# Optimization experiments

Hardware: AMD Instinct MI355X
Metric: run time of the kernel (lower is better)

Reference implementation:

```python
import jax, jax.numpy as jnp
import numpy as np

MIDC = 128
HEADS = 4
HEADC = MIDC // HEADS
EPS = 1e-5


def _layernorm(x, w, b):
    # Faithful to the custom torch LayerNorm: unbiased std (ddof=1) and (std + eps) in denominator.
    mean = jnp.mean(x, axis=-1, keepdims=True)
    std = jnp.std(x, axis=-1, keepdims=True, ddof=1)
    return w * ((x - mean) / (std + EPS)) + b


def setup_inputs() -> dict:
    key = jax.random.key(0)
    ks = jax.random.split(key, 8)
    B, C, D, H, W = 2, MIDC, 16, 64, 64
    s = 1.0 / np.sqrt(C)
    return {
        "x": jax.random.normal(ks[0], (B, C, D, H, W), dtype=jnp.float32),
        "qkv_w": jax.random.normal(ks[1], (3 * C, C), dtype=jnp.float32) * s,
        "qkv_b": jnp.zeros((3 * C,), dtype=jnp.float32),
        "o1_w": jax.random.normal(ks[2], (C, C), dtype=jnp.float32) * s,
        "o1_b": jnp.zeros((C,), dtype=jnp.float32),
        "o2_w": jax.random.normal(ks[3], (C, C), dtype=jnp.float32) * s,
        "o2_b": jnp.zeros((C,), dtype=jnp.float32),
        "kln_w": jnp.ones((HEADS, 1, HEADC), dtype=jnp.float32),
        "kln_b": jnp.zeros((HEADS, 1, HEADC), dtype=jnp.float32),
        "vln_w": jnp.ones((HEADS, 1, HEADC), dtype=jnp.float32),
        "vln_b": jnp.zeros((HEADS, 1, HEADC), dtype=jnp.float32),
    }


def reference(x, qkv_w, qkv_b, o1_w, o1_b, o2_w, o2_b, kln_w, kln_b, vln_w, vln_b):
    B, C, D, H, W = x.shape
    heads, headc = HEADS, HEADC
    bias = x
    # 1x1x1 Conv3d == pointwise linear over channel dim
    qkv = jnp.einsum('bcdhw,oc->bdhwo', x, qkv_w) + qkv_b          # [B,D,H,W,3C]
    qkv = qkv.reshape(B * D, H * W, heads, 3 * headc)
    qkv = qkv.transpose(0, 2, 1, 3)                                 # [BD,heads,HW,3hc]
    q, k, v = jnp.split(qkv, 3, axis=-1)                            # each [BD,heads,HW,hc]
    k = _layernorm(k, kln_w, kln_b)
    v = _layernorm(v, vln_w, vln_b)
    # linear attention: (K^T V) then Q (K^T V)
    kv = jnp.einsum('bhnc,bhnd->bhcd', k, v) / (H * W)              # [BD,heads,hc,hc]
    v = jnp.einsum('bhnc,bhcd->bhnd', q, kv)                        # [BD,heads,HW,hc]
    v = v.transpose(0, 2, 1, 3).reshape(B, D, H, W, C)
    ret = v.transpose(0, 4, 1, 2, 3) + bias                         # [B,C,D,H,W]
    h = jnp.einsum('bcdhw,oc->bodhw', ret, o1_w) + o1_b[None, :, None, None, None]
    h = jax.nn.gelu(h, approximate=False)
    out = jnp.einsum('bcdhw,oc->bodhw', h, o2_w) + o2_b[None, :, None, None, None]
    return out + bias
```

## Files before the change

### kernel.cpp

```cpp
#include <hip/hip_runtime.h>
#include <cmath>

typedef float  f32x4  __attribute__((ext_vector_type(4)));
typedef __bf16 bf16x8 __attribute__((ext_vector_type(8)));
typedef __bf16 bf16x4 __attribute__((ext_vector_type(4)));

#define MFMA16(acc, a, b) (acc) = __builtin_amdgcn_mfma_f32_16x16x32_bf16((a), (b), (acc), 0, 0, 0)


__device__ __forceinline__ int swz(int row, int colByte){ return row*256 + (colByte ^ ((row & 7) << 4)); }
__device__ __forceinline__ int swzP(int row, int colByte){ return row*128 + (colByte ^ ((row & 7) << 4)); }

__device__ __forceinline__ void loadx(float* sx, const float* __restrict__ xb, int t){
  int p = t & 63, cg = t >> 6;
  const float* col = xb + p;
  #pragma unroll
  for (int i = 0; i < 4; ++i)
    #pragma unroll
    for (int j = 0; j < 8; ++j)
      sx[i*8 + j] = col[(cg*8 + i*32 + j) * 65536];
}
__device__ __forceinline__ void writex(const float* sx, char* ldsX, int t){
  int p = t & 63, cg = t >> 6;
  #pragma unroll
  for (int i = 0; i < 4; ++i){
    bf16x8 u;
    #pragma unroll
    for (int j = 0; j < 8; ++j) u[j] = (__bf16)sx[i*8 + j];
    *(bf16x8*)(ldsX + swz(p, cg*16 + i*64)) = u;
  }
}

__global__ __launch_bounds__(256) void wprep(const float* __restrict__ qkv_w,
                                             const float* __restrict__ o1w,
                                             const float* __restrict__ o2w,
                                             __bf16* __restrict__ w16){
  int e = (blockIdx.x * 256 + threadIdx.x) * 4;
  const float* src; int off;
  if (e < 49152)      { src = qkv_w; off = e; }
  else if (e < 65536) { src = o1w;   off = e - 49152; }
  else                { src = o2w;   off = e - 65536; }
  f32x4 v = *(const f32x4*)(src + off);
  bf16x4 o;
  #pragma unroll
  for (int r = 0; r < 4; ++r) o[r] = (__bf16)v[r];
  *(bf16x4*)(w16 + e) = o;
}

__global__ __launch_bounds__(256, 5) void k1_kv(
    const float* __restrict__ x, const __bf16* __restrict__ w16, const float* __restrict__ qkv_b,
    const float* __restrict__ klw, const float* __restrict__ klb,
    const float* __restrict__ vlw, const float* __restrict__ vlb,
    float* __restrict__ kvacc){
  __shared__ char ldsX[16384];
  __shared__ char ksS[4][4096];
  int t = threadIdx.x, lane = t & 63, w = t >> 6, l15 = lane & 15, l4 = lane >> 4;
  int bx = blockIdx.x, bd = bx >> 6, b = bd >> 4, d = bd & 15;
  const float* xb = x + (size_t)b*8388608 + d*4096 + (bx & 63)*64;

  float sx[32];
  loadx(sx, xb, t);
  writex(sx, ldsX, t);
  __syncthreads();

  char* ks = ksS[w];
  f32x4 accv[2][4];
  #pragma unroll
  for (int ph = 0; ph < 2; ++ph){
    int po = 96*w + 32 + 32*ph;
    f32x4 acc[2][4] = {};
    #pragma unroll
    for (int kf = 0; kf < 4; ++kf){
      bf16x8 a0 = *(const bf16x8*)(w16 + (po + l15)*128 + kf*32 + l4*8);
      bf16x8 a1 = *(const bf16x8*)(w16 + (po + 16 + l15)*128 + kf*32 + l4*8);
      bf16x8 bn0 = *(const bf16x8*)(ldsX + swz(l15,      kf*64 + l4*16));
      bf16x8 bn1 = *(const bf16x8*)(ldsX + swz(16 + l15, kf*64 + l4*16));
      bf16x8 bn2 = *(const bf16x8*)(ldsX + swz(32 + l15, kf*64 + l4*16));
      bf16x8 bn3 = *(const bf16x8*)(ldsX + swz(48 + l15, kf*64 + l4*16));
      MFMA16(acc[0][0], a0, bn0); MFMA16(acc[0][1], a0, bn1);
      MFMA16(acc[0][2], a0, bn2); MFMA16(acc[0][3], a0, bn3);
      MFMA16(acc[1][0], a1, bn0); MFMA16(acc[1][1], a1, bn1);
      MFMA16(acc[1][2], a1, bn2); MFMA16(acc[1][3], a1, bn3);
    }
    const float* lwp = (ph ? vlw : klw) + 32*w;
    const float* lbp = (ph ? vlb : klb) + 32*w;
    f32x4 b0  = *(const f32x4*)(qkv_b + po + l4*4);
    f32x4 b1  = *(const f32x4*)(qkv_b + po + 16 + l4*4);
    f32x4 lw0 = *(const f32x4*)(lwp + l4*4), lw1 = *(const f32x4*)(lwp + 16 + l4*4);
    f32x4 lb0 = *(const f32x4*)(lbp + l4*4), lb1 = *(const f32x4*)(lbp + 16 + l4*4);
    #pragma unroll
    for (int n = 0; n < 4; ++n){
      f32x4 v0 = acc[0][n] + b0;
      f32x4 v1 = acc[1][n] + b1;
      float s1 = v0[0]+v0[1]+v0[2]+v0[3] + v1[0]+v1[1]+v1[2]+v1[3];
      float s2 = v0[0]*v0[0]+v0[1]*v0[1]+v0[2]*v0[2]+v0[3]*v0[3]
               + v1[0]*v1[0]+v1[1]*v1[1]+v1[2]*v1[2]+v1[3]*v1[3];
      s1 += __shfl_xor(s1, 16); s2 += __shfl_xor(s2, 16);
      s1 += __shfl_xor(s1, 32); s2 += __shfl_xor(s2, 32);
      float m   = s1 * (1.f/32.f);
      float var = fmaxf((s2 - 32.f*m*m) * (1.f/31.f), 0.f);
      float inv = 1.f / (sqrtf(var) + 1e-5f);
      v0 = (v0 - m) * inv * lw0 + lb0;
      v1 = (v1 - m) * inv * lw1 + lb1;
      if (ph == 0){
        int pB = (16*n + l15) * 2;
        #pragma unroll
        for (int r = 0; r < 4; ++r){
          *(__bf16*)(ks + swzP(l4*4 + r, pB))      = (__bf16)v0[r];
          *(__bf16*)(ks + swzP(16 + l4*4 + r, pB)) = (__bf16)v1[r];
        }
      } else {
        accv[0][n] = v0; accv[1][n] = v1;
      }
    }
  }
  __syncthreads();
  char* vs = ldsX + w * 4096;
  #pragma unroll
  for (int n = 0; n < 4; ++n){
    int pB = (16*n + l15) * 2;
    #pragma unroll
    for (int r = 0; r < 4; ++r){
      *(__bf16*)(vs + swzP(l4*4 + r, pB))      = (__bf16)accv[0][n][r];
      *(__bf16*)(vs + swzP(16 + l4*4 + r, pB)) = (__bf16)accv[1][n][r];
    }
  }
  f32x4 kv[2][2] = {};
  #pragma unroll
  for (int kf = 0; kf < 2; ++kf){
    bf16x8 av0 = *(const bf16x8*)(vs + swzP(l15,      kf*64 + l4*16));
    bf16x8 av1 = *(const bf16x8*)(vs + swzP(16 + l15, kf*64 + l4*16));
    bf16x8 bk0 = *(const bf16x8*)(ks + swzP(l15,      kf*64 + l4*16));
    bf16x8 bk1 = *(const bf16x8*)(ks + swzP(16 + l15, kf*64 + l4*16));
    MFMA16(kv[0][0], av0, bk0); MFMA16(kv[0][1], av0, bk1);
    MFMA16(kv[1][0], av1, bk0); MFMA16(kv[1][1], av1, bk1);
  }
  float* kh = kvacc + ((size_t)bd*4 + w)*1024;
  #pragma unroll
  for (int m = 0; m < 2; ++m)
    #pragma unroll
    for (int n = 0; n < 2; ++n)
      #pragma unroll
      for (int r = 0; r < 4; ++r)
        atomicAdd(kh + (16*m + l4*4 + r)*32 + 16*n + l15, kv[m][n][r] * (1.f/4096.f));
}

__global__ __launch_bounds__(256, 5) void k2_main(
    const float* __restrict__ x, const __bf16* __restrict__ w16, const float* __restrict__ qkv_b,
    const float* __restrict__ o1b, const float* __restrict__ o2b,
    const float* __restrict__ kvacc, float* __restrict__ out){
  __shared__ char lx[16384];
  __shared__ char wk[16384];
  int t = threadIdx.x, lane = t & 63, w = t >> 6, l15 = lane & 15, l4 = lane >> 4;
  int bx = blockIdx.x, bd = bx >> 6, b = bd >> 4, d = bd & 15;
  size_t gofs = (size_t)b*8388608 + d*4096 + (bx & 63)*64;
  const float* xb = x + gofs;
  float* ob = out + gofs;
  const __bf16* w1 = w16 + 49152;
  const __bf16* w2 = w16 + 65536;
  int oo = 32 * w;

  float sx[32];
  loadx(sx, xb, t);
  const float* kvh = kvacc + ((size_t)bd*4 + w)*1024;
  f32x4 ql0 = *(const f32x4*)(kvh + l15*32 + l4*8);
  f32x4 qh0 = *(const f32x4*)(kvh + l15*32 + l4*8 + 4);
  f32x4 ql1 = *(const f32x4*)(kvh + (16 + l15)*32 + l4*8);
  f32x4 qh1 = *(const f32x4*)(kvh + (16 + l15)*32 + l4*8 + 4);
  writex(sx, lx, t);
  bf16x8 ka0, ka1;
  #pragma unroll
  for (int j = 0; j < 4; ++j){
    ka0[j] = (__bf16)ql0[j]; ka0[j+4] = (__bf16)qh0[j];
    ka1[j] = (__bf16)ql1[j]; ka1[j+4] = (__bf16)qh1[j];
  }
  __syncthreads();

  {
    f32x4 acc[2][4] = {};
    #pragma unroll
    for (int kf = 0; kf < 4; ++kf){
      bf16x8 a0 = *(const bf16x8*)(w16 + (96*w + l15)*128 + kf*32 + l4*8);
      bf16x8 a1 = *(const bf16x8*)(w16 + (96*w + 16 + l15)*128 + kf*32 + l4*8);
      bf16x8 bn0 = *(const bf16x8*)(lx + swz(l15,      kf*64 + l4*16));
      bf16x8 bn1 = *(const bf16x8*)(lx + swz(16 + l15, kf*64 + l4*16));
      bf16x8 bn2 = *(const bf16x8*)(lx + swz(32 + l15, kf*64 + l4*16));
      bf16x8 bn3 = *(const bf16x8*)(lx + swz(48 + l15, kf*64 + l4*16));
      MFMA16(acc[0][0], a0, bn0); MFMA16(acc[0][1], a0, bn1);
      MFMA16(acc[0][2], a0, bn2); MFMA16(acc[0][3], a0, bn3);
      MFMA16(acc[1][0], a1, bn0); MFMA16(acc[1][1], a1, bn1);
      MFMA16(acc[1][2], a1, bn2); MFMA16(acc[1][3], a1, bn3);
    }
    #pragma unroll
    for (int m = 0; m < 2; ++m){
      f32x4 qb = *(const f32x4*)(qkv_b + 96*w + 16*m + l4*4);
      int cB = (oo + 16*m + l4*4) * 2;
      #pragma unroll
      for (int n = 0; n < 4; ++n){
        bf16x4 pk;
        #pragma unroll
        for (int r = 0; r < 4; ++r) pk[r] = (__bf16)(acc[m][n][r] + qb[r]);
        *(bf16x4*)(wk + swz(16*n + l15, cB)) = pk;
      }
    }
  }
  {
    f32x4 acc[2][4] = {};
    #pragma unroll
    for (int n = 0; n < 4; ++n){
      bf16x8 bq = *(const bf16x8*)(wk + swz(16*n + l15, oo*2 + l4*16));
      MFMA16(acc[0][n], ka0, bq);
      MFMA16(acc[1][n], ka1, bq);
    }
    #pragma unroll
    for (int m = 0; m < 2; ++m){
      int cB = (oo + 16*m + l4*4) * 2;
      #pragma unroll
      for (int n = 0; n < 4; ++n){
        bf16x4 xv = *(const bf16x4*)(lx + swz(16*n + l15, cB));
        bf16x4 pk;
        #pragma unroll
        for (int r = 0; r < 4; ++r) pk[r] = (__bf16)(acc[m][n][r] + (float)xv[r]);
        *(bf16x4*)(wk + swz(16*n + l15, cB)) = pk;
      }
    }
  }
  __syncthreads();

  f32x4 acc1[2][4] = {};
  #pragma unroll
  for (int kf = 0; kf < 4; ++kf){
    bf16x8 a0 = *(const bf16x8*)(w1 + (oo + l15)*128 + kf*32 + l4*8);
    bf16x8 a1 = *(const bf16x8*)(w1 + (oo + 16 + l15)*128 + kf*32 + l4*8);
    bf16x8 bn0 = *(const bf16x8*)(wk + swz(l15,      kf*64 + l4*16));
    bf16x8 bn1 = *(const bf16x8*)(wk + swz(16 + l15, kf*64 + l4*16));
    bf16x8 bn2 = *(const bf16x8*)(wk + swz(32 + l15, kf*64 + l4*16));
    bf16x8 bn3 = *(const bf16x8*)(wk + swz(48 + l15, kf*64 + l4*16));
    MFMA16(acc1[0][0], a0, bn0); MFMA16(acc1[0][1], a0, bn1);
    MFMA16(acc1[0][2], a0, bn2); MFMA16(acc1[0][3], a0, bn3);
    MFMA16(acc1[1][0], a1, bn0); MFMA16(acc1[1][1], a1, bn1);
    MFMA16(acc1[1][2], a1, bn2); MFMA16(acc1[1][3], a1, bn3);
  }
  __syncthreads();
  #pragma unroll
  for (int m = 0; m < 2; ++m){
    f32x4 bb = *(const f32x4*)(o1b + oo + 16*m + l4*4);
    int cB = (oo + 16*m + l4*4) * 2;
    #pragma unroll
    for (int n = 0; n < 4; ++n){
      bf16x4 pk;
      #pragma unroll
      for (int r = 0; r < 4; ++r){
        float v = acc1[m][n][r] + bb[r];
        float z = v * (1.5957691216f + 0.0713548164f * v * v);
        float g = v / (1.f + __expf(-z));
        pk[r] = (__bf16)g;
      }
      *(bf16x4*)(wk + swz(16*n + l15, cB)) = pk;
    }
  }
  __syncthreads();

  f32x4 acc2[2][4] = {};
  #pragma unroll
  for (int kf = 0; kf < 4; ++kf){
    bf16x8 a0 = *(const bf16x8*)(w2 + (oo + l15)*128 + kf*32 + l4*8);
    bf16x8 a1 = *(const bf16x8*)(w2 + (oo + 16 + l15)*128 + kf*32 + l4*8);
    bf16x8 bn0 = *(const bf16x8*)(wk + swz(l15,      kf*64 + l4*16));
    bf16x8 bn1 = *(const bf16x8*)(wk + swz(16 + l15, kf*64 + l4*16));
    bf16x8 bn2 = *(const bf16x8*)(wk + swz(32 + l15, kf*64 + l4*16));
    bf16x8 bn3 = *(const bf16x8*)(wk + swz(48 + l15, kf*64 + l4*16));
    MFMA16(acc2[0][0], a0, bn0); MFMA16(acc2[0][1], a0, bn1);
    MFMA16(acc2[0][2], a0, bn2); MFMA16(acc2[0][3], a0, bn3);
    MFMA16(acc2[1][0], a1, bn0); MFMA16(acc2[1][1], a1, bn1);
    MFMA16(acc2[1][2], a1, bn2); MFMA16(acc2[1][3], a1, bn3);
  }
  #pragma unroll
  for (int m = 0; m < 2; ++m){
    int c0 = oo + 16*m + l4*4;
    f32x4 bb = *(const f32x4*)(o2b + c0);
    #pragma unroll
    for (int n = 0; n < 4; ++n){
      bf16x4 xv = *(const bf16x4*)(lx + swz(16*n + l15, c0*2));
      #pragma unroll
      for (int r = 0; r < 4; ++r)
        ob[(size_t)(c0 + r)*65536 + 16*n + l15] = acc2[m][n][r] + bb[r] + (float)xv[r];
    }
  }
}

extern "C" void kernel_launch(void* const* d_in, const int* in_sizes, int n_in,
                              void* d_out, int out_size, void* d_ws, size_t ws_size,
                              hipStream_t stream){
  const float* x     = (const float*)d_in[0];
  const float* qkv_w = (const float*)d_in[1];
  const float* qkv_b = (const float*)d_in[2];
  const float* o1w   = (const float*)d_in[3];
  const float* o1b   = (const float*)d_in[4];
  const float* o2w   = (const float*)d_in[5];
  const float* o2b   = (const float*)d_in[6];
  const float* klw   = (const float*)d_in[7];
  const float* klb   = (const float*)d_in[8];
  const float* vlw   = (const float*)d_in[9];
  const float* vlb   = (const float*)d_in[10];

  float*  kvacc = (float*)d_ws;
  __bf16* w16   = (__bf16*)((char*)d_ws + 524288);

  hipMemsetAsync(kvacc, 0, (size_t)32 * 4096 * 4, stream);
  wprep<<<80, 256, 0, stream>>>(qkv_w, o1w, o2w, w16);
  k1_kv<<<2048, 256, 0, stream>>>(x, w16, qkv_b, klw, klb, vlw, vlb, kvacc);
  k2_main<<<2048, 256, 0, stream>>>(x, w16, qkv_b, o1b, o2b, kvacc, (float*)d_out);
}
```

Measured before the change: 106.9 us.

## Replace atomic KV accumulation with bf16 partials and separate reduction kernel

k1 now handles two 64-position chunks per block, prefetching the second chunk's x into registers while the first is computed. It writes per-block bf16 partial KV matrices instead of issuing global float atomics, and a new reduce kernel sums the 32 partials per slice, which also removes the memset. Weight fragments are preloaded into registers before the MFMA loops in both kernels, and the GELU pass is computed before the barrier so it overlaps. The costs are an extra kernel launch, about 8 MB of partial traffic, and lower precision from storing partials in bf16.

After: 118.0 us. 10.3% more time.

```diff
diff --git a/kernel.cpp b/kernel.cpp
--- a/kernel.cpp
+++ b/kernel.cpp
@@ -4,6 +4,7 @@
 typedef float  f32x4  __attribute__((ext_vector_type(4)));
 typedef __bf16 bf16x8 __attribute__((ext_vector_type(8)));
 typedef __bf16 bf16x4 __attribute__((ext_vector_type(4)));
+typedef __bf16 bf16x2 __attribute__((ext_vector_type(2)));
 
 #define MFMA16(acc, a, b) (acc) = __builtin_amdgcn_mfma_f32_16x16x32_bf16((a), (b), (acc), 0, 0, 0)
 
@@ -51,104 +52,134 @@
     const float* __restrict__ x, const __bf16* __restrict__ w16, const float* __restrict__ qkv_b,
     const float* __restrict__ klw, const float* __restrict__ klb,
     const float* __restrict__ vlw, const float* __restrict__ vlb,
-    float* __restrict__ kvacc){
+    __bf16* __restrict__ part){
   __shared__ char ldsX[16384];
   __shared__ char ksS[4][4096];
   int t = threadIdx.x, lane = t & 63, w = t >> 6, l15 = lane & 15, l4 = lane >> 4;
-  int bx = blockIdx.x, bd = bx >> 6, b = bd >> 4, d = bd & 15;
-  const float* xb = x + (size_t)b*8388608 + d*4096 + (bx & 63)*64;
+  int bx = blockIdx.x, bd = bx >> 5, b = bd >> 4, d = bd & 15;
+  const float* xb = x + (size_t)b*8388608 + d*4096 + (bx & 31)*128;
+  char* ks = ksS[w];
+  char* vs = ldsX + w * 4096;
+  f32x4 kv[2][2] = {};
 
   float sx[32];
   loadx(sx, xb, t);
   writex(sx, ldsX, t);
   __syncthreads();
-
-  char* ks = ksS[w];
-  f32x4 accv[2][4];
-  #pragma unroll
-  for (int ph = 0; ph < 2; ++ph){
-    int po = 96*w + 32 + 32*ph;
-    f32x4 acc[2][4] = {};
-    #pragma unroll
-    for (int kf = 0; kf < 4; ++kf){
-      bf16x8 a0 = *(const bf16x8*)(w16 + (po + l15)*128 + kf*32 + l4*8);
-      bf16x8 a1 = *(const bf16x8*)(w16 + (po + 16 + l15)*128 + kf*32 + l4*8);
-      bf16x8 bn0 = *(const bf16x8*)(ldsX + swz(l15,      kf*64 + l4*16));
-      bf16x8 bn1 = *(const bf16x8*)(ldsX + swz(16 + l15, kf*64 + l4*16));
-      bf16x8 bn2 = *(const bf16x8*)(ldsX + swz(32 + l15, kf*64 + l4*16));
-      bf16x8 bn3 = *(const bf16x8*)(ldsX + swz(48 + l15, kf*64 + l4*16));
-      MFMA16(acc[0][0], a0, bn0); MFMA16(acc[0][1], a0, bn1);
-      MFMA16(acc[0][2], a0, bn2); MFMA16(acc[0][3], a0, bn3);
-      MFMA16(acc[1][0], a1, bn0); MFMA16(acc[1][1], a1, bn1);
-      MFMA16(acc[1][2], a1, bn2); MFMA16(acc[1][3], a1, bn3);
-    }
-    const float* lwp = (ph ? vlw : klw) + 32*w;
-    const float* lbp = (ph ? vlb : klb) + 32*w;
-    f32x4 b0  = *(const f32x4*)(qkv_b + po + l4*4);
-    f32x4 b1  = *(const f32x4*)(qkv_b + po + 16 + l4*4);
-    f32x4 lw0 = *(const f32x4*)(lwp + l4*4), lw1 = *(const f32x4*)(lwp + 16 + l4*4);
-    f32x4 lb0 = *(const f32x4*)(lbp + l4*4), lb1 = *(const f32x4*)(lbp + 16 + l4*4);
+  float sx2[32];
+  loadx(sx2, xb + 64, t);
+
+  #pragma unroll
+  for (int ch = 0; ch < 2; ++ch){
+    if (ch == 1){
+      __syncthreads();
+      writex(sx2, ldsX, t);
+      __syncthreads();
+    }
+    f32x4 accv[2][4];
+    #pragma unroll
+    for (int ph = 0; ph < 2; ++ph){
+      int po = 96*w + 32 + 32*ph;
+      bf16x8 A0[4], A1[4];
+      #pragma unroll
+      for (int kf = 0; kf < 4; ++kf){
+        A0[kf] = *(const bf16x8*)(w16 + (po + l15)*128 + kf*32 + l4*8);
+        A1[kf] = *(const bf16x8*)(w16 + (po + 16 + l15)*128 + kf*32 + l4*8);
+      }
+      f32x4 acc[2][4] = {};
+      #pragma unroll
+      for (int kf = 0; kf < 4; ++kf){
+        bf16x8 bn0 = *(const bf16x8*)(ldsX + swz(l15,      kf*64 + l4*16));
+        bf16x8 bn1 = *(const bf16x8*)(ldsX + swz(16 + l15, kf*64 + l4*16));
+        bf16x8 bn2 = *(const bf16x8*)(ldsX + swz(32 + l15, kf*64 + l4*16));
+        bf16x8 bn3 = *(const bf16x8*)(ldsX + swz(48 + l15, kf*64 + l4*16));
+        MFMA16(acc[0][0], A0[kf], bn0); MFMA16(acc[0][1], A0[kf], bn1);
+        MFMA16(acc[0][2], A0[kf], bn2); MFMA16(acc[0][3], A0[kf], bn3);
+        MFMA16(acc[1][0], A1[kf], bn0); MFMA16(acc[1][1], A1[kf], bn1);
+        MFMA16(acc[1][2], A1[kf], bn2); MFMA16(acc[1][3], A1[kf], bn3);
+      }
+      const float* lwp = (ph ? vlw : klw) + 32*w;
+      const float* lbp = (ph ? vlb : klb) + 32*w;
+      f32x4 b0  = *(const f32x4*)(qkv_b + po + l4*4);
+      f32x4 b1  = *(const f32x4*)(qkv_b + po + 16 + l4*4);
+      f32x4 lw0 = *(const f32x4*)(lwp + l4*4), lw1 = *(const f32x4*)(lwp + 16 + l4*4);
+      f32x4 lb0 = *(const f32x4*)(lbp + l4*4), lb1 = *(const f32x4*)(lbp + 16 + l4*4);
+      #pragma unroll
+      for (int n = 0; n < 4; ++n){
+        f32x4 v0 = acc[0][n] + b0;
+        f32x4 v1 = acc[1][n] + b1;
+        float s1 = v0[0]+v0[1]+v0[2]+v0[3] + v1[0]+v1[1]+v1[2]+v1[3];
+        float s2 = v0[0]*v0[0]+v0[1]*v0[1]+v0[2]*v0[2]+v0[3]*v0[3]
+                 + v1[0]*v1[0]+v1[1]*v1[1]+v1[2]*v1[2]+v1[3]*v1[3];
+        s1 += __shfl_xor(s1, 16); s2 += __shfl_xor(s2, 16);
+        s1 += __shfl_xor(s1, 32); s2 += __shfl_xor(s2, 32);
+        float m   = s1 * (1.f/32.f);
+        float var = fmaxf((s2 - 32.f*m*m) * (1.f/31.f), 0.f);
+        float inv = 1.f / (sqrtf(var) + 1e-5f);
+        v0 = (v0 - m) * inv * lw0 + lb0;
+        v1 = (v1 - m) * inv * lw1 + lb1;
+        if (ph == 0){
+          int pB = (16*n + l15) * 2;
+          #pragma unroll
+          for (int r = 0; r < 4; ++r){
+            *(__bf16*)(ks + swzP(l4*4 + r, pB))      = (__bf16)v0[r];
+            *(__bf16*)(ks + swzP(16 + l4*4 + r, pB)) = (__bf16)v1[r];
+          }
+        } else {
+          accv[0][n] = v0; accv[1][n] = v1;
+        }
+      }
+    }
+    __syncthreads();
     #pragma unroll
     for (int n = 0; n < 4; ++n){
-      f32x4 v0 = acc[0][n] + b0;
-      f32x4 v1 = acc[1][n] + b1;
-      float s1 = v0[0]+v0[1]+v0[2]+v0[3] + v1[0]+v1[1]+v1[2]+v1[3];
-      float s2 = v0[0]*v0[0]+v0[1]*v0[1]+v0[2]*v0[2]+v0[3]*v0[3]
-               + v1[0]*v1[0]+v1[1]*v1[1]+v1[2]*v1[2]+v1[3]*v1[3];
-      s1 += __shfl_xor(s1, 16); s2 += __shfl_xor(s2, 16);
-      s1 += __shfl_xor(s1, 32); s2 += __shfl_xor(s2, 32);
-      float m   = s1 * (1.f/32.f);
-      float var = fmaxf((s2 - 32.f*m*m) * (1.f/31.f), 0.f);
-      float inv = 1.f / (sqrtf(var) + 1e-5f);
-      v0 = (v0 - m) * inv * lw0 + lb0;
-      v1 = (v1 - m) * inv * lw1 + lb1;
-      if (ph == 0){
-        int pB = (16*n + l15) * 2;
-        #pragma unroll
-        for (int r = 0; r < 4; ++r){
-          *(__bf16*)(ks + swzP(l4*4 + r, pB))      = (__bf16)v0[r];
-          *(__bf16*)(ks + swzP(16 + l4*4 + r, pB)) = (__bf16)v1[r];
-        }
-      } else {
-        accv[0][n] = v0; accv[1][n] = v1;
-      }
-    }
-  }
-  __syncthreads();
-  char* vs = ldsX + w * 4096;
-  #pragma unroll
-  for (int n = 0; n < 4; ++n){
-    int pB = (16*n + l15) * 2;
-    #pragma unroll
-    for (int r = 0; r < 4; ++r){
-      *(__bf16*)(vs + swzP(l4*4 + r, pB))      = (__bf16)accv[0][n][r];
-      *(__bf16*)(vs + swzP(16 + l4*4 + r, pB)) = (__bf16)accv[1][n][r];
-    }
-  }
-  f32x4 kv[2][2] = {};
-  #pragma unroll
-  for (int kf = 0; kf < 2; ++kf){
-    bf16x8 av0 = *(const bf16x8*)(vs + swzP(l15,      kf*64 + l4*16));
-    bf16x8 av1 = *(const bf16x8*)(vs + swzP(16 + l15, kf*64 + l4*16));
-    bf16x8 bk0 = *(const bf16x8*)(ks + swzP(l15,      kf*64 + l4*16));
-    bf16x8 bk1 = *(const bf16x8*)(ks + swzP(16 + l15, kf*64 + l4*16));
-    MFMA16(kv[0][0], av0, bk0); MFMA16(kv[0][1], av0, bk1);
-    MFMA16(kv[1][0], av1, bk0); MFMA16(kv[1][1], av1, bk1);
-  }
-  float* kh = kvacc + ((size_t)bd*4 + w)*1024;
+      int pB = (16*n + l15) * 2;
+      #pragma unroll
+      for (int r = 0; r < 4; ++r){
+        *(__bf16*)(vs + swzP(l4*4 + r, pB))      = (__bf16)accv[0][n][r];
+        *(__bf16*)(vs + swzP(16 + l4*4 + r, pB)) = (__bf16)accv[1][n][r];
+      }
+    }
+    #pragma unroll
+    for (int kf = 0; kf < 2; ++kf){
+      bf16x8 av0 = *(const bf16x8*)(vs + swzP(l15,      kf*64 + l4*16));
+      bf16x8 av1 = *(const bf16x8*)(vs + swzP(16 + l15, kf*64 + l4*16));
+      bf16x8 bk0 = *(const bf16x8*)(ks + swzP(l15,      kf*64 + l4*16));
+      bf16x8 bk1 = *(const bf16x8*)(ks + swzP(16 + l15, kf*64 + l4*16));
+      MFMA16(kv[0][0], av0, bk0); MFMA16(kv[0][1], av0, bk1);
+      MFMA16(kv[1][0], av1, bk0); MFMA16(kv[1][1], av1, bk1);
+    }
+  }
+
+  __bf16* pb = part + (size_t)bx*4096 + w*1024;
   #pragma unroll
   for (int m = 0; m < 2; ++m)
     #pragma unroll
     for (int n = 0; n < 2; ++n)
       #pragma unroll
       for (int r = 0; r < 4; ++r)
-        atomicAdd(kh + (16*m + l4*4 + r)*32 + 16*n + l15, kv[m][n][r] * (1.f/4096.f));
+        pb[(16*m + l4*4 + r)*32 + 16*n + l15] = (__bf16)kv[m][n][r];
+}
+
+__global__ __launch_bounds__(256) void k15_reduce(const __bf16* __restrict__ part,
+                                                  float* __restrict__ kvt){
+  int bx = blockIdx.x, t = threadIdx.x;
+  int bd = bx >> 3, seg = bx & 7;
+  int e = seg * 512 + t * 2;
+  float s0 = 0.f, s1 = 0.f;
+  #pragma unroll
+  for (int sub = 0; sub < 32; ++sub){
+    bf16x2 p = *(const bf16x2*)(part + (size_t)(bd * 32 + sub) * 4096 + e);
+    s0 += (float)p[0]; s1 += (float)p[1];
+  }
+  kvt[bd * 4096 + e]     = s0 * (1.f / 4096.f);
+  kvt[bd * 4096 + e + 1] = s1 * (1.f / 4096.f);
 }
 
 __global__ __launch_bounds__(256, 5) void k2_main(
     const float* __restrict__ x, const __bf16* __restrict__ w16, const float* __restrict__ qkv_b,
     const float* __restrict__ o1b, const float* __restrict__ o2b,
-    const float* __restrict__ kvacc, float* __restrict__ out){
+    const float* __restrict__ kvt, float* __restrict__ out){
   __shared__ char lx[16384];
   __shared__ char wk[16384];
   int t = threadIdx.x, lane = t & 63, w = t >> 6, l15 = lane & 15, l4 = lane >> 4;
@@ -162,7 +193,7 @@
 
   float sx[32];
   loadx(sx, xb, t);
-  const float* kvh = kvacc + ((size_t)bd*4 + w)*1024;
+  const float* kvh = kvt + ((size_t)bd*4 + w)*1024;
   f32x4 ql0 = *(const f32x4*)(kvh + l15*32 + l4*8);
   f32x4 qh0 = *(const f32x4*)(kvh + l15*32 + l4*8 + 4);
   f32x4 ql1 = *(const f32x4*)(kvh + (16 + l15)*32 + l4*8);
@@ -177,19 +208,23 @@
   __syncthreads();
 
   {
+    bf16x8 A0[4], A1[4];
+    #pragma unroll
+    for (int kf = 0; kf < 4; ++kf){
+      A0[kf] = *(const bf16x8*)(w16 + (96*w + l15)*128 + kf*32 + l4*8);
+      A1[kf] = *(const bf16x8*)(w16 + (96*w + 16 + l15)*128 + kf*32 + l4*8);
+    }
     f32x4 acc[2][4] = {};
     #pragma unroll
     for (int kf = 0; kf < 4; ++kf){
-      bf16x8 a0 = *(const bf16x8*)(w16 + (96*w + l15)*128 + kf*32 + l4*8);
-      bf16x8 a1 = *(const bf16x8*)(w16 + (96*w + 16 + l15)*128 + kf*32 + l4*8);
       bf16x8 bn0 = *(const bf16x8*)(lx + swz(l15,      kf*64 + l4*16));
       bf16x8 bn1 = *(const bf16x8*)(lx + swz(16 + l15, kf*64 + l4*16));
       bf16x8 bn2 = *(const bf16x8*)(lx + swz(32 + l15, kf*64 + l4*16));
       bf16x8 bn3 = *(const bf16x8*)(lx + swz(48 + l15, kf*64 + l4*16));
-      MFMA16(acc[0][0], a0, bn0); MFMA16(acc[0][1], a0, bn1);
-      MFMA16(acc[0][2], a0, bn2); MFMA16(acc[0][3], a0, bn3);
-      MFMA16(acc[1][0], a1, bn0); MFMA16(acc[1][1], a1, bn1);
-      MFMA16(acc[1][2], a1, bn2); MFMA16(acc[1][3], a1, bn3);
+      MFMA16(acc[0][0], A0[kf], bn0); MFMA16(acc[0][1], A0[kf], bn1);
+      MFMA16(acc[0][2], A0[kf], bn2); MFMA16(acc[0][3], A0[kf], bn3);
+      MFMA16(acc[1][0], A1[kf], bn0); MFMA16(acc[1][1], A1[kf], bn1);
+      MFMA16(acc[1][2], A1[kf], bn2); MFMA16(acc[1][3], A1[kf], bn3);
     }
     #pragma unroll
     for (int m = 0; m < 2; ++m){
@@ -227,64 +262,79 @@
   }
   __syncthreads();
 
-  f32x4 acc1[2][4] = {};
-  #pragma unroll
-  for (int kf = 0; kf < 4; ++kf){
-    bf16x8 a0 = *(const bf16x8*)(w1 + (oo + l15)*128 + kf*32 + l4*8);
-    bf16x8 a1 = *(const bf16x8*)(w1 + (oo + 16 + l15)*128 + kf*32 + l4*8);
-    bf16x8 bn0 = *(const bf16x8*)(wk + swz(l15,      kf*64 + l4*16));
-    bf16x8 bn1 = *(const bf16x8*)(wk + swz(16 + l15, kf*64 + l4*16));
-    bf16x8 bn2 = *(const bf16x8*)(wk + swz(32 + l15, kf*64 + l4*16));
-    bf16x8 bn3 = *(const bf16x8*)(wk + swz(48 + l15, kf*64 + l4*16));
-    MFMA16(acc1[0][0], a0, bn0); MFMA16(acc1[0][1], a0, bn1);
-    MFMA16(acc1[0][2], a0, bn2); MFMA16(acc1[0][3], a0, bn3);
-    MFMA16(acc1[1][0], a1, bn0); MFMA16(acc1[1][1], a1, bn1);
-    MFMA16(acc1[1][2], a1, bn2); MFMA16(acc1[1][3], a1, bn3);
+  {
+    bf16x8 A0[4], A1[4];
+    #pragma unroll
+    for (int kf = 0; kf < 4; ++kf){
+      A0[kf] = *(const bf16x8*)(w1 + (oo + l15)*128 + kf*32 + l4*8);
+      A1[kf] = *(const bf16x8*)(w1 + (oo + 16 + l15)*128 + kf*32 + l4*8);
+    }
+    f32x4 acc1[2][4] = {};
+    #pragma unroll
+    for (int kf = 0; kf < 4; ++kf){
+      bf16x8 bn0 = *(const bf16x8*)(wk + swz(l15,      kf*64 + l4*16));
+      bf16x8 bn1 = *(const bf16x8*)(wk + swz(16 + l15, kf*64 + l4*16));
+      bf16x8 bn2 = *(const bf16x8*)(wk + swz(32 + l15, kf*64 + l4*16));
+      bf16x8 bn3 = *(const bf16x8*)(wk + swz(48 + l15, kf*64 + l4*16));
+      MFMA16(acc1[0][0], A0[kf], bn0); MFMA16(acc1[0][1], A0[kf], bn1);
+      MFMA16(acc1[0][2], A0[kf], bn2); MFMA16(acc1[0][3], A0[kf], bn3);
+      MFMA16(acc1[1][0], A1[kf], bn0); MFMA16(acc1[1][1], A1[kf], bn1);
+      MFMA16(acc1[1][2], A1[kf], bn2); MFMA16(acc1[1][3], A1[kf], bn3);
+    }
+    bf16x4 hk[2][4];
+    #pragma unroll
+    for (int m = 0; m < 2; ++m){
+      f32x4 bb = *(const f32x4*)(o1b + oo + 16*m + l4*4);
+      #pragma unroll
+      for (int n = 0; n < 4; ++n)
+        #pragma unroll
+        for (int r = 0; r < 4; ++r){
+          float v = acc1[m][n][r] + bb[r];
+          float z = v * (1.5957691216f + 0.0713548164f * v * v);
+          hk[m][n][r] = (__bf16)(v / (1.f + __expf(-z)));
+        }
+    }
+    __syncthreads();
+    #pragma unroll
+    for (int m = 0; m < 2; ++m){
+      int cB = (oo + 16*m + l4*4) * 2;
+      #pragma unroll
+      for (int n = 0; n < 4; ++n)
+        *(bf16x4*)(wk + swz(16*n + l15, cB)) = hk[m][n];
+    }
   }
   __syncthreads();
-  #pragma unroll
-  for (int m = 0; m < 2; ++m){
-    f32x4 bb = *(const f32x4*)(o1b + oo + 16*m + l4*4);
-    int cB = (oo + 16*m + l4*4) * 2;
-    #pragma unroll
-    for (int n = 0; n < 4; ++n){
-      bf16x4 pk;
-      #pragma unroll
-      for (int r = 0; r < 4; ++r){
-        float v = acc1[m][n][r] + bb[r];
-        float z = v * (1.5957691216f + 0.0713548164f * v * v);
-        float g = v / (1.f + __expf(-z));
-        pk[r] = (__bf16)g;
-      }
-      *(bf16x4*)(wk + swz(16*n + l15, cB)) = pk;
-    }
-  }
-  __syncthreads();
-
-  f32x4 acc2[2][4] = {};
-  #pragma unroll
-  for (int kf = 0; kf < 4; ++kf){
-    bf16x8 a0 = *(const bf16x8*)(w2 + (oo + l15)*128 + kf*32 + l4*8);
-    bf16x8 a1 = *(const bf16x8*)(w2 + (oo + 16 + l15)*128 + kf*32 + l4*8);
-    bf16x8 bn0 = *(const bf16x8*)(wk + swz(l15,      kf*64 + l4*16));
-    bf16x8 bn1 = *(const bf16x8*)(wk + swz(16 + l15, kf*64 + l4*16));
-    bf16x8 bn2 = *(const bf16x8*)(wk + swz(32 + l15, kf*64 + l4*16));
-    bf16x8 bn3 = *(const bf16x8*)(wk + swz(48 + l15, kf*64 + l4*16));
-    MFMA16(acc2[0][0], a0, bn0); MFMA16(acc2[0][1], a0, bn1);
-    MFMA16(acc2[0][2], a0, bn2); MFMA16(acc2[0][3], a0, bn3);
-    MFMA16(acc2[1][0], a1, bn0); MFMA16(acc2[1][1], a1, bn1);
-    MFMA16(acc2[1][2], a1, bn2); MFMA16(acc2[1][3], a1, bn3);
-  }
-  #pragma unroll
-  for (int m = 0; m < 2; ++m){
-    int c0 = oo + 16*m + l4*4;
-    f32x4 bb = *(const f32x4*)(o2b + c0);
-    #pragma unroll
-    for (int n = 0; n < 4; ++n){
-      bf16x4 xv = *(const bf16x4*)(lx + swz(16*n + l15, c0*2));
-      #pragma unroll
-      for (int r = 0; r < 4; ++r)
-        ob[(size_t)(c0 + r)*65536 + 16*n + l15] = acc2[m][n][r] + bb[r] + (float)xv[r];
+
+  {
+    bf16x8 A0[4], A1[4];
+    #pragma unroll
+    for (int kf = 0; kf < 4; ++kf){
+      A0[kf] = *(const bf16x8*)(w2 + (oo + l15)*128 + kf*32 + l4*8);
+      A1[kf] = *(const bf16x8*)(w2 + (oo + 16 + l15)*128 + kf*32 + l4*8);
+    }
+    f32x4 acc2[2][4] = {};
+    #pragma unroll
+    for (int kf = 0; kf < 4; ++kf){
+      bf16x8 bn0 = *(const bf16x8*)(wk + swz(l15,      kf*64 + l4*16));
+      bf16x8 bn1 = *(const bf16x8*)(wk + swz(16 + l15, kf*64 + l4*16));
+      bf16x8 bn2 = *(const bf16x8*)(wk + swz(32 + l15, kf*64 + l4*16));
+      bf16x8 bn3 = *(const bf16x8*)(wk + swz(48 + l15, kf*64 + l4*16));
+      MFMA16(acc2[0][0], A0[kf], bn0); MFMA16(acc2[0][1], A0[kf], bn1);
+      MFMA16(acc2[0][2], A0[kf], bn2); MFMA16(acc2[0][3], A0[kf], bn3);
+      MFMA16(acc2[1][0], A1[kf], bn0); MFMA16(acc2[1][1], A1[kf], bn1);
+      MFMA16(acc2[1][2], A1[kf], bn2); MFMA16(acc2[1][3], A1[kf], bn3);
+    }
+    #pragma unroll
+    for (int m = 0; m < 2; ++m){
+      int c0 = oo + 16*m + l4*4;
+      f32x4 bb = *(const f32x4*)(o2b + c0);
+      #pragma unroll
+      for (int n = 0; n < 4; ++n){
+        bf16x4 xv = *(const bf16x4*)(lx + swz(16*n + l15, c0*2));
+        #pragma unroll
+        for (int r = 0; r < 4; ++r)
+          ob[(size_t)(c0 + r)*65536 + 16*n + l15] = acc2[m][n][r] + bb[r] + (float)xv[r];
+      }
     }
   }
 }
@@ -304,11 +354,12 @@
   const float* vlw   = (const float*)d_in[9];
   const float* vlb   = (const float*)d_in[10];
 
-  float*  kvacc = (float*)d_ws;
-  __bf16* w16   = (__bf16*)((char*)d_ws + 524288);
-
-  hipMemsetAsync(kvacc, 0, (size_t)32 * 4096 * 4, stream);
+  __bf16* part = (__bf16*)d_ws;
+  float*  kvt  = (float*)((char*)d_ws + 8388608);
+  __bf16* w16  = (__bf16*)((char*)d_ws + 8912896);
+
   wprep<<<80, 256, 0, stream>>>(qkv_w, o1w, o2w, w16);
-  k1_kv<<<2048, 256, 0, stream>>>(x, w16, qkv_b, klw, klb, vlw, vlb, kvacc);
-  k2_main<<<2048, 256, 0, stream>>>(x, w16, qkv_b, o1b, o2b, kvacc, (float*)d_out);
-}
+  k1_kv<<<1024, 256, 0, stream>>>(x, w16, qkv_b, klw, klb, vlw, vlb, part);
+  k15_reduce<<<256, 256, 0, stream>>>(part, kvt);
+  k2_main<<<2048, 256, 0, stream>>>(x, w16, qkv_b, o1b, o2b, kvt, (float*)d_out);
+}
```
